# Optimization experiments

Measured on AMD Instinct MI355X. Metric: run time of the kernel, lower is better.

Reference implementation:

```python
import jax, jax.numpy as jnp
import numpy as np

NUM_CLASSES = 32
N = 2_000_000
EPS = jnp.float32(np.finfo(np.float32).eps)  # torch.finfo(torch.float32).eps


def setup_inputs() -> dict:
    key = jax.random.key(0)
    k1, k2 = jax.random.split(key)
    y_true = jax.random.normal(k1, (N, NUM_CLASSES), dtype=jnp.float32)
    y_pred = jax.random.normal(k2, (N, NUM_CLASSES), dtype=jnp.float32)
    confusion_matrix = jnp.zeros((NUM_CLASSES, NUM_CLASSES), dtype=jnp.float32)
    return {"y_true": y_true, "y_pred": y_pred, "confusion_matrix": confusion_matrix}


def reference(y_true, y_pred, confusion_matrix):
    C = confusion_matrix.shape[0]
    # update(): argmax then scatter-accumulate into the confusion matrix
    t = jnp.argmax(y_true, axis=1)  # [N] int
    p = jnp.argmax(y_pred, axis=1)  # [N] int
    flat = t * C + p                # flattened (row, col) index
    hist = jnp.zeros((C * C,), dtype=jnp.float32).at[flat].add(1.0)
    cm = confusion_matrix + hist.reshape(C, C)
    # compute() with average='macro'
    tp = jnp.diag(cm)
    predicted_positives = jnp.sum(cm, axis=0)
    precision_per_class = tp / (predicted_positives + EPS)
    return jnp.mean(precision_per_class)
```

## Files before the change

kernel.cpp:

```cpp
#include <hip/hip_runtime.h>

#define C 32
#define BINS (C * C)
#define NBLOCKS 2048
#define NTHREADS 256
#define GROUP_STRIDE ((NBLOCKS * NTHREADS) / 8)
#define STRIDE2 (2 * GROUP_STRIDE)
#define FLT_EPS 1.1920928955078125e-07f

typedef float v4f __attribute__((ext_vector_type(4)));

template <int CTRL>
__device__ __forceinline__ float dpp_maxf(float x) {
    float o = __int_as_float(__builtin_amdgcn_update_dpp(
        0, __float_as_int(x), CTRL, 0xF, 0xF, true));
    return fmaxf(x, o);
}
template <int CTRL>
__device__ __forceinline__ unsigned int dpp_minu(unsigned int x) {
    unsigned int o = (unsigned int)__builtin_amdgcn_update_dpp(
        0, (int)x, CTRL, 0xF, 0xF, true);
    return x < o ? x : o;
}

__device__ __forceinline__ int group_argmax(v4f v, int base) {
    float m = fmaxf(fmaxf(v.x, v.y), fmaxf(v.z, v.w));
    m = dpp_maxf<0xB1>(m);
    m = dpp_maxf<0x4E>(m);
    m = dpp_maxf<0x141>(m);
    unsigned int idx = 255u;
    idx = (v.w == m) ? (unsigned int)(base + 3) : idx;
    idx = (v.z == m) ? (unsigned int)(base + 2) : idx;
    idx = (v.y == m) ? (unsigned int)(base + 1) : idx;
    idx = (v.x == m) ? (unsigned int)(base + 0) : idx;
    idx = dpp_minu<0xB1>(idx);
    idx = dpp_minu<0x4E>(idx);
    idx = dpp_minu<0x141>(idx);
    return (int)idx;
}

__global__ __launch_bounds__(NTHREADS) void hist_kernel(
    const float* __restrict__ yt,
    const float* __restrict__ yp,
    unsigned int* __restrict__ partial,
    int N)
{
    __shared__ unsigned int lhist[BINS];
    const int t = threadIdx.x;
    for (int i = t; i < BINS; i += NTHREADS) lhist[i] = 0u;
    __syncthreads();

    const int lane8 = t & 7;
    const int base = lane8 * 4;
    const float* pt = yt + base;
    const float* pp = yp + base;

    long long r0 = (long long)((blockIdx.x * NTHREADS + t) >> 3);
    long long r1 = r0 + GROUP_STRIDE;
    bool v0 = r0 < N;
    bool v1 = r1 < N;
    v4f a0, b0, a1, b1;
    if (v0) {
        a0 = __builtin_nontemporal_load((const v4f*)(pt + r0 * C));
        b0 = __builtin_nontemporal_load((const v4f*)(pp + r0 * C));
    }
    if (v1) {
        a1 = __builtin_nontemporal_load((const v4f*)(pt + r1 * C));
        b1 = __builtin_nontemporal_load((const v4f*)(pp + r1 * C));
    }

    while (v0) {
        const long long n0 = r0 + STRIDE2;
        const long long n1 = r1 + STRIDE2;
        const bool nv0 = n0 < N;
        const bool nv1 = n1 < N;
        v4f na0, nb0, na1, nb1;
        if (nv0) {
            na0 = __builtin_nontemporal_load((const v4f*)(pt + n0 * C));
            nb0 = __builtin_nontemporal_load((const v4f*)(pp + n0 * C));
        }
        if (nv1) {
            na1 = __builtin_nontemporal_load((const v4f*)(pt + n1 * C));
            nb1 = __builtin_nontemporal_load((const v4f*)(pp + n1 * C));
        }

        const int ti0 = group_argmax(a0, base);
        const int pi0 = group_argmax(b0, base);
        if (lane8 == 0) atomicAdd(&lhist[ti0 * C + pi0], 1u);
        if (v1) {
            const int ti1 = group_argmax(a1, base);
            const int pi1 = group_argmax(b1, base);
            if (lane8 == 1) atomicAdd(&lhist[ti1 * C + pi1], 1u);
        }

        r0 = n0; r1 = n1; v0 = nv0; v1 = nv1;
        a0 = na0; b0 = nb0; a1 = na1; b1 = nb1;
    }

    __syncthreads();
    if (t < 32) {
        unsigned int cs = 0;
        #pragma unroll
        for (int i = 0; i < C; ++i) cs += lhist[i * C + t];
        partial[(size_t)blockIdx.x * 64 + t] = cs;
    } else if (t < 64) {
        const int j = t - 32;
        partial[(size_t)blockIdx.x * 64 + t] = lhist[j * C + j];
    }
}

__global__ __launch_bounds__(1024) void finalize_kernel(
    const unsigned int* __restrict__ partial,
    const float* __restrict__ cm_in,
    float* __restrict__ out)
{
    __shared__ float sums[16][64];
    const int tid = threadIdx.x;
    const int col = tid & 63;
    const int kg = tid >> 6;

    unsigned int s = 0;
    #pragma unroll 8
    for (int k = kg * (NBLOCKS / 16); k < (kg + 1) * (NBLOCKS / 16); ++k)
        s += partial[(size_t)k * 64 + col];
    sums[kg][col] = (float)s;
    __syncthreads();

    if (tid < 64) {
        float tot = 0.0f;
        #pragma unroll
        for (int g = 0; g < 16; ++g) tot += sums[g][tid];
        sums[0][tid] = tot;
    }
    __syncthreads();

    if (tid < C) {
        const int j = tid;
        float pp = sums[0][j];
        float tp = sums[0][C + j];
        float cmcol = 0.0f;
        #pragma unroll
        for (int i = 0; i < C; ++i) cmcol += cm_in[i * C + j];
        pp += cmcol;
        tp += cm_in[j * C + j];
        float prec = tp / (pp + FLT_EPS);
        #pragma unroll
        for (int m = 1; m < C; m <<= 1) prec += __shfl_xor(prec, m);
        if (j == 0) out[0] = prec * (1.0f / (float)C);
    }
}

extern "C" void kernel_launch(void* const* d_in, const int* in_sizes, int n_in,
                              void* d_out, int out_size, void* d_ws, size_t ws_size,
                              hipStream_t stream)
{
    const float* yt = (const float*)d_in[0];
    const float* yp = (const float*)d_in[1];
    const float* cm = (const float*)d_in[2];
    float* out = (float*)d_out;
    const int N = in_sizes[0] / C;

    unsigned int* partial = (unsigned int*)d_ws;

    hist_kernel<<<NBLOCKS, NTHREADS, 0, stream>>>(yt, yp, partial, N);
    finalize_kernel<<<1, 1024, 0, stream>>>(partial, cm, out);
}
```

Baseline: 461.5 us.

## Assign contiguous row chunks per block and drop nontemporal loads

Each block now processes its own contiguous chunk of rows, rounded to a multiple of 64, instead of grid-striding across the whole matrix. Addressing uses 32-bit offsets from a per-block base pointer. The nontemporal loads are replaced with ordinary vector loads. The aim is better DRAM page and prefetch locality and cheaper address arithmetic, at the risk of load imbalance at the tail and a change in cache behaviour from dropping the nontemporal hints.

```diff
diff --git a/kernel.cpp b/kernel.cpp
--- a/kernel.cpp
+++ b/kernel.cpp
@@ -4,8 +4,6 @@
 #define BINS (C * C)
 #define NBLOCKS 2048
 #define NTHREADS 256
-#define GROUP_STRIDE ((NBLOCKS * NTHREADS) / 8)
-#define STRIDE2 (2 * GROUP_STRIDE)
 #define FLT_EPS 1.1920928955078125e-07f
 
 typedef float v4f __attribute__((ext_vector_type(4)));
@@ -43,7 +41,7 @@
     const float* __restrict__ yt,
     const float* __restrict__ yp,
     unsigned int* __restrict__ partial,
-    int N)
+    int N, int chunk)
 {
     __shared__ unsigned int lhist[BINS];
     const int t = threadIdx.x;
@@ -52,36 +50,39 @@
 
     const int lane8 = t & 7;
     const int base = lane8 * 4;
-    const float* pt = yt + base;
-    const float* pp = yp + base;
+    const int g = t >> 3;
 
-    long long r0 = (long long)((blockIdx.x * NTHREADS + t) >> 3);
-    long long r1 = r0 + GROUP_STRIDE;
-    bool v0 = r0 < N;
-    bool v1 = r1 < N;
+    const long long row_lo = (long long)blockIdx.x * chunk;
+    const long long row_hi_ll = row_lo + chunk;
+    const int nrows = (int)((row_hi_ll < N ? row_hi_ll : (long long)N) - row_lo) > 0
+                    ? (int)((row_hi_ll < N ? row_hi_ll : (long long)N) - row_lo) : 0;
+
+    const float* bt = yt + row_lo * C;
+    const float* bp = yp + row_lo * C;
+
+    int r0 = g;
+    int r1 = g + 32;
+    unsigned int off = (unsigned int)(r0 * C + base);
+    bool v0 = r0 < nrows;
+    bool v1 = r1 < nrows;
     v4f a0, b0, a1, b1;
-    if (v0) {
-        a0 = __builtin_nontemporal_load((const v4f*)(pt + r0 * C));
-        b0 = __builtin_nontemporal_load((const v4f*)(pp + r0 * C));
-    }
-    if (v1) {
-        a1 = __builtin_nontemporal_load((const v4f*)(pt + r1 * C));
-        b1 = __builtin_nontemporal_load((const v4f*)(pp + r1 * C));
-    }
+    if (v0) { a0 = *(const v4f*)(bt + off);          b0 = *(const v4f*)(bp + off); }
+    if (v1) { a1 = *(const v4f*)(bt + off + 32 * C); b1 = *(const v4f*)(bp + off + 32 * C); }
 
     while (v0) {
-        const long long n0 = r0 + STRIDE2;
-        const long long n1 = r1 + STRIDE2;
-        const bool nv0 = n0 < N;
-        const bool nv1 = n1 < N;
+        const int n0 = r0 + 64;
+        const int n1 = r1 + 64;
+        const bool nv0 = n0 < nrows;
+        const bool nv1 = n1 < nrows;
+        const unsigned int noff = off + 64 * C;
         v4f na0, nb0, na1, nb1;
         if (nv0) {
-            na0 = __builtin_nontemporal_load((const v4f*)(pt + n0 * C));
-            nb0 = __builtin_nontemporal_load((const v4f*)(pp + n0 * C));
+            na0 = *(const v4f*)(bt + noff);
+            nb0 = *(const v4f*)(bp + noff);
         }
         if (nv1) {
-            na1 = __builtin_nontemporal_load((const v4f*)(pt + n1 * C));
-            nb1 = __builtin_nontemporal_load((const v4f*)(pp + n1 * C));
+            na1 = *(const v4f*)(bt + noff + 32 * C);
+            nb1 = *(const v4f*)(bp + noff + 32 * C);
         }
 
         const int ti0 = group_argmax(a0, base);
@@ -93,7 +94,7 @@
             if (lane8 == 1) atomicAdd(&lhist[ti1 * C + pi1], 1u);
         }
 
-        r0 = n0; r1 = n1; v0 = nv0; v1 = nv1;
+        r0 = n0; r1 = n1; v0 = nv0; v1 = nv1; off = noff;
         a0 = na0; b0 = nb0; a1 = na1; b1 = nb1;
     }
 
@@ -160,8 +161,10 @@
     float* out = (float*)d_out;
     const int N = in_sizes[0] / C;
 
+    const int chunk = (((N + NBLOCKS - 1) / NBLOCKS) + 63) & ~63;
+
     unsigned int* partial = (unsigned int*)d_ws;
 
-    hist_kernel<<<NBLOCKS, NTHREADS, 0, stream>>>(yt, yp, partial, N);
+    hist_kernel<<<NBLOCKS, NTHREADS, 0, stream>>>(yt, yp, partial, N, chunk);
     finalize_kernel<<<1, 1024, 0, stream>>>(partial, cm, out);
 }
```

Measured after the change: 491.9 us. 1.07x slower.
